# Performance work log

Measured on AMD Instinct MI355X. Metric: run time of the kernel, lower is better.

The kernel has to match this reference:

```python
import jax, jax.numpy as jnp
import numpy as np

IN_C = 256
INTER_C = 128  # in_channels // reduction_ratio


def setup_inputs() -> dict:
    key = jax.random.key(0)
    ks = jax.random.split(key, 9)
    s = 1.0 / np.sqrt(IN_C)
    si = 1.0 / np.sqrt(INTER_C)
    return {
        "x": jax.random.normal(ks[0], (8, IN_C, 64, 64), dtype=jnp.float32),
        "g_w": jax.random.uniform(ks[1], (INTER_C, IN_C), jnp.float32, -s, s),
        "g_b": jax.random.uniform(ks[2], (INTER_C,), jnp.float32, -s, s),
        "theta_w": jax.random.uniform(ks[3], (INTER_C, IN_C), jnp.float32, -s, s),
        "theta_b": jax.random.uniform(ks[4], (INTER_C,), jnp.float32, -s, s),
        "phi_w": jax.random.uniform(ks[5], (INTER_C, IN_C), jnp.float32, -s, s),
        "phi_b": jax.random.uniform(ks[6], (INTER_C,), jnp.float32, -s, s),
        "W_w": jax.random.uniform(ks[7], (IN_C, INTER_C), jnp.float32, -si, si),
        "W_b": jax.random.uniform(ks[8], (IN_C,), jnp.float32, -si, si),
    }


def _conv1x1(x, w, b):
    # x: [b, cin, h, w]; w: [cout, cin] -> [b, cout, h, w]
    return jnp.einsum('oc,bchw->bohw', w, x) + b[None, :, None, None]


def reference(x, g_w, g_b, theta_w, theta_b, phi_w, phi_b, W_w, W_b):
    b, c, h, w = x.shape
    n = h * w
    g_x = _conv1x1(x, g_w, g_b).reshape(b, INTER_C, n)        # [b, i, n]
    theta_x = _conv1x1(x, theta_w, theta_b).reshape(b, INTER_C, n)
    phi_x = _conv1x1(x, phi_w, phi_b).reshape(b, INTER_C, n)
    # f[b, q, k] = sum_i theta[b, i, q] * phi[b, i, k]
    f = jnp.einsum('biq,bik->bqk', theta_x, phi_x)            # [b, n, n]
    f_div_C = jax.nn.softmax(f, axis=-1)
    # y[b, q, i] = sum_k f_div_C[b, q, k] * g_x[b, i, k]
    y = jnp.einsum('bqk,bik->biq', f_div_C, g_x)              # [b, i, n]
    y = y.reshape(b, INTER_C, h, w)
    W_y = _conv1x1(y, W_w, W_b)
    return W_y + x
```

## Files before the change

### kernel.cpp

```cpp
#include <hip/hip_runtime.h>
#include <hip/hip_bf16.h>
#include <stdint.h>

#define NB 8
#define CIN 256
#define IC 128
#define NP 4096

typedef __attribute__((ext_vector_type(8))) short s8v;
typedef __attribute__((ext_vector_type(4))) short s4v;
typedef __attribute__((ext_vector_type(16))) float f16v;
typedef __attribute__((ext_vector_type(4))) float f4v;

#define MFMA32(a, b, c) __builtin_amdgcn_mfma_f32_32x32x16_bf16(a, b, c, 0, 0, 0)

__device__ __forceinline__ unsigned short f2bf(float f) {
  union { float f; unsigned int u; } v; v.f = f;
  unsigned int u = v.u;
  return (unsigned short)((u + 0x7FFFu + ((u >> 16) & 1u)) >> 16);
}

__device__ __forceinline__ unsigned short f2bf_h(float f) {
  __hip_bfloat16 h = __float2bfloat16(f);
  union { __hip_bfloat16 h; unsigned short u; } cv; cv.h = h;
  return cv.u;
}

__device__ __forceinline__ float bf2f(short s) {
  union { unsigned int u; float f; } cv;
  cv.u = ((unsigned int)(unsigned short)s) << 16;
  return cv.f;
}

typedef const unsigned int __attribute__((address_space(1))) gas_u32;
typedef unsigned int __attribute__((address_space(3))) las_u32;
__device__ __forceinline__ void gload_lds16(const void* g, void* l) {
  __builtin_amdgcn_global_load_lds((gas_u32*)g, (las_u32*)l, 16, 0, 0);
}

__global__ __launch_bounds__(256) void k_wprep(const float* __restrict__ thw,
    const float* __restrict__ phw, const float* __restrict__ gw,
    const float* __restrict__ Ww, unsigned short* __restrict__ wB) {
  const int g = blockIdx.x >> 5;
  const int base = (blockIdx.x & 31) * 1024 + threadIdx.x * 4;
  const float* src = (g == 0) ? thw : ((g == 1) ? phw : ((g == 2) ? gw : Ww));
  const float sc = (g == 0) ? 1.44269504f : 1.0f;
  const f4v v = *(const f4v*)(src + base);
  ushort4 u;
  u.x = f2bf(v[0] * sc); u.y = f2bf(v[1] * sc);
  u.z = f2bf(v[2] * sc); u.w = f2bf(v[3] * sc);
  *(ushort4*)(wB + g * 32768 + base) = u;
}

__global__ __launch_bounds__(256) void k_conv3(const float* __restrict__ x,
    const unsigned short* __restrict__ wB,
    const float* __restrict__ thb, const float* __restrict__ phb,
    const float* __restrict__ gb,
    unsigned short* __restrict__ Qg, unsigned short* __restrict__ Kg,
    unsigned short* __restrict__ Vtg) {
  __shared__ unsigned short X[64 * 256];
  __shared__ unsigned short T[64][72];
  const int t = threadIdx.x, lane = t & 63, wid = t >> 6;
  const int b = blockIdx.x & 7;
  const int p0 = (blockIdx.x >> 3) * 64;
  const int hl = lane >> 5;
  const float* xb = x + (size_t)b * CIN * NP + p0;
  const int cl = t >> 4;
  const int p4 = (t & 15) * 4;
  for (int sub = 0; sub < 4; ++sub) {
    const int c0 = sub * 64;
#pragma unroll
    for (int j = 0; j < 4; ++j) {
      const int cloc = cl + j * 16;
      const f4v v = *(const f4v*)(xb + (size_t)(c0 + cloc) * NP + p4);
      ushort4 u;
      u.x = f2bf(v[0]); u.y = f2bf(v[1]); u.z = f2bf(v[2]); u.w = f2bf(v[3]);
      *(ushort4*)&T[cloc][p4 ^ ((cloc & 7) * 8)] = u;
    }
    __syncthreads();
    const int p = t >> 2;
#pragma unroll
    for (int half = 0; half < 2; ++half) {
      const int cg = (t & 3) + half * 4;
      alignas(16) unsigned short outv[8];
#pragma unroll
      for (int k = 0; k < 8; ++k)
        outv[k] = T[cg * 8 + k][p ^ (k * 8)];
      const int cc = sub * 8 + cg;
      *(uint4*)&X[p * 256 + 8 * (cc ^ (2 * (p & 15)))] = *(const uint4*)outv;
    }
    __syncthreads();
  }
  const int orow = wid * 32 + (lane & 31);

  for (int mat = 0; mat < 3; ++mat) {
    const unsigned short* WB = wB + mat * 32768;
    const float* Bs = (mat == 0) ? thb : ((mat == 1) ? phb : gb);
    const float wsc = (mat == 0) ? 1.44269504f : 1.0f;
    s8v wf[16];
#pragma unroll
    for (int s = 0; s < 16; ++s)
      wf[s] = *(const s8v*)&WB[(size_t)orow * CIN + hl * 8 + 16 * s];
    float br[16];
#pragma unroll
    for (int r = 0; r < 16; ++r)
      br[r] = Bs[wid * 32 + (r & 3) + 8 * (r >> 2) + 4 * hl] * wsc;

#pragma unroll
    for (int nt = 0; nt < 2; ++nt) {
      const int p = (lane & 31) + nt * 32;
      f16v acc;
#pragma unroll
      for (int i = 0; i < 16; ++i) acc[i] = 0.f;
#pragma unroll
      for (int s = 0; s < 16; ++s) {
        const int cc0 = hl + 2 * s;
        const s8v xf = *(const s8v*)&X[p * 256 + 8 * (cc0 ^ (2 * (p & 15)))];
        acc = MFMA32(wf[s], xf, acc);
      }
      if (mat < 2) {
        unsigned short* G = ((mat == 0) ? Qg : Kg) + ((size_t)b * NP + p0 + p) * IC;
#pragma unroll
        for (int grp = 0; grp < 4; ++grp) {
          const int d0 = wid * 32 + 8 * grp + 4 * hl;
          ushort4 u;
          u.x = f2bf(acc[grp * 4 + 0] + br[grp * 4 + 0]);
          u.y = f2bf(acc[grp * 4 + 1] + br[grp * 4 + 1]);
          u.z = f2bf(acc[grp * 4 + 2] + br[grp * 4 + 2]);
          u.w = f2bf(acc[grp * 4 + 3] + br[grp * 4 + 3]);
          *(ushort4*)(G + d0) = u;
        }
      } else {
        unsigned short* G = Vtg + (size_t)b * IC * NP + p0 + p;
#pragma unroll
        for (int r = 0; r < 16; ++r) {
          const int row = wid * 32 + (r & 3) + 8 * (r >> 2) + 4 * hl;
          G[(size_t)row * NP] = f2bf(acc[r] + br[r]);
        }
      }
    }
  }
}

__global__ __launch_bounds__(256, 2) void k_attn(const unsigned short* __restrict__ Qg,
    const unsigned short* __restrict__ Kg, const unsigned short* __restrict__ Vtg,
    unsigned short* __restrict__ Opart, float2* __restrict__ stats) {
  __shared__ unsigned short Klds[2][64 * 128];
  __shared__ unsigned short Vlds[2][128 * 64];
  const int t = threadIdx.x, lane = t & 63, wid = t >> 6;
  const int bid = blockIdx.x;
  const int b = bid & 7;
  const int q0 = ((bid >> 3) & 31) * 128;
  const int half = bid >> 8;
  const int it0 = half * 32;
  const int hl = lane >> 5;
  const int q = q0 + wid * 32 + (lane & 31);
  const unsigned short* Qp = Qg + (size_t)b * NP * IC + (size_t)q * IC;
  s8v qf[8];
#pragma unroll
  for (int s = 0; s < 8; ++s)
    qf[s] = *(const s8v*)(Qp + hl * 8 + 16 * s);
  f16v oa[4];
#pragma unroll
  for (int dt = 0; dt < 4; ++dt)
#pragma unroll
    for (int i = 0; i < 16; ++i) oa[dt][i] = 0.f;
  float m = -3.0e38f, lsum = 0.f;
  const unsigned short* Kb = Kg + (size_t)b * NP * IC;
  const unsigned short* Vb = Vtg + (size_t)b * IC * NP;
  const int vrow_l = lane >> 3;
  const int vchunk = 8 * ((lane & 7) ^ vrow_l);

#pragma unroll
  for (int r = 0; r < 4; ++r) {
    const int ci = wid * 256 + r * 64 + lane;
    const int kv = ci >> 4, cc = ci & 15;
    gload_lds16(Kb + (size_t)(it0 * 64 + kv) * IC + 8 * (cc ^ (kv & 15)),
                (char*)&Klds[0][0] + wid * 4096 + r * 1024);
  }
#pragma unroll
  for (int r = 0; r < 4; ++r) {
    const int d = 32 * wid + 8 * r + vrow_l;
    gload_lds16(Vb + (size_t)d * NP + it0 * 64 + vchunk,
                (char*)&Vlds[0][0] + (32 * wid + 8 * r) * 128);
  }
  __syncthreads();

  for (int it = it0; it < it0 + 32; ++it) {
    const int cur = it & 1;
    const bool more = (it < it0 + 31);
    if (more) {
      const int kv0n = (it + 1) * 64;
#pragma unroll
      for (int r = 0; r < 4; ++r) {
        const int ci = wid * 256 + r * 64 + lane;
        const int kv = ci >> 4, cc = ci & 15;
        gload_lds16(Kb + (size_t)(kv0n + kv) * IC + 8 * (cc ^ (kv & 15)),
                    (char*)&Klds[cur ^ 1][0] + wid * 4096 + r * 1024);
      }
#pragma unroll
      for (int r = 0; r < 4; ++r) {
        const int d = 32 * wid + 8 * r + vrow_l;
        gload_lds16(Vb + (size_t)d * NP + kv0n + vchunk,
                    (char*)&Vlds[cur ^ 1][0] + (32 * wid + 8 * r) * 128);
      }
    }
    f16v st0a, st0b, st1a, st1b;
#pragma unroll
    for (int i = 0; i < 16; ++i) { st0a[i] = 0.f; st0b[i] = 0.f; st1a[i] = 0.f; st1b[i] = 0.f; }
    const int kva = lane & 31;
    __builtin_amdgcn_s_setprio(1);
#pragma unroll
    for (int s = 0; s < 8; s += 2) {
      const int cc0 = hl + 2 * s;
      const s8v ka0 = *(const s8v*)&Klds[cur][kva * 128 + 8 * (cc0 ^ (kva & 15))];
      const s8v kb0 = *(const s8v*)&Klds[cur][(kva + 32) * 128 + 8 * (cc0 ^ (kva & 15))];
      const s8v ka1 = *(const s8v*)&Klds[cur][kva * 128 + 8 * ((cc0 + 2) ^ (kva & 15))];
      const s8v kb1 = *(const s8v*)&Klds[cur][(kva + 32) * 128 + 8 * ((cc0 + 2) ^ (kva & 15))];
      st0a = MFMA32(ka0, qf[s], st0a);
      st1a = MFMA32(kb0, qf[s], st1a);
      st0b = MFMA32(ka1, qf[s + 1], st0b);
      st1b = MFMA32(kb1, qf[s + 1], st1b);
    }
    __builtin_amdgcn_s_setprio(0);
    f16v st0 = st0a + st0b;
    f16v st1 = st1a + st1b;
    float tm[16];
#pragma unroll
    for (int i = 0; i < 16; ++i) tm[i] = fmaxf(st0[i], st1[i]);
#pragma unroll
    for (int w = 8; w >= 1; w >>= 1)
#pragma unroll
      for (int i = 0; i < 16; ++i) if (i < w) tm[i] = fmaxf(tm[i], tm[i + w]);
    float pmax = fmaxf(tm[0], __shfl_xor(tm[0], 32));
    if (__any(pmax > m + 8.f)) {
      const float mn = fmaxf(m, pmax);
      const float sc = __builtin_amdgcn_exp2f(m - mn);
      m = mn;
      lsum *= sc;
#pragma unroll
      for (int dt = 0; dt < 4; ++dt)
#pragma unroll
        for (int i = 0; i < 16; ++i) oa[dt][i] *= sc;
    }
#pragma unroll
    for (int i = 0; i < 16; ++i) st0[i] = __builtin_amdgcn_exp2f(st0[i] - m);
#pragma unroll
    for (int i = 0; i < 16; ++i) st1[i] = __builtin_amdgcn_exp2f(st1[i] - m);
    float ts[16];
#pragma unroll
    for (int i = 0; i < 16; ++i) ts[i] = st0[i] + st1[i];
#pragma unroll
    for (int w = 8; w >= 1; w >>= 1)
#pragma unroll
      for (int i = 0; i < 16; ++i) if (i < w) ts[i] += ts[i + w];
    lsum += ts[0] + __shfl_xor(ts[0], 32);
    s8v pf0, pf1, pf2, pf3;
#pragma unroll
    for (int i = 0; i < 8; ++i) {
      pf0[i] = (short)f2bf_h(st0[i]);
      pf1[i] = (short)f2bf_h(st0[8 + i]);
      pf2[i] = (short)f2bf_h(st1[i]);
      pf3[i] = (short)f2bf_h(st1[8 + i]);
    }
    __builtin_amdgcn_s_setprio(1);
#pragma unroll
    for (int ks = 0; ks < 4; ++ks) {
      const s8v pcur = (ks == 0) ? pf0 : ((ks == 1) ? pf1 : ((ks == 2) ? pf2 : pf3));
      const int c0 = 2 * (ks & 1) + 4 * (ks >> 1);
#pragma unroll
      for (int dt = 0; dt < 4; ++dt) {
        const int d = dt * 32 + (lane & 31);
        const int dj = (lane & 31) & 7;
        const s4v va  = *(const s4v*)&Vlds[cur][d * 64 + 8 * (c0 ^ dj) + 4 * hl];
        const s4v vb2 = *(const s4v*)&Vlds[cur][d * 64 + 8 * ((c0 + 1) ^ dj) + 4 * hl];
        s8v vf;
        vf[0] = va[0]; vf[1] = va[1]; vf[2] = va[2]; vf[3] = va[3];
        vf[4] = vb2[0]; vf[5] = vb2[1]; vf[6] = vb2[2]; vf[7] = vb2[3];
        oa[dt] = MFMA32(vf, pcur, oa[dt]);
      }
    }
    __builtin_amdgcn_s_setprio(0);
    __syncthreads();
  }
  const float inv = 1.0f / lsum;
  unsigned short* Op = Opart + (size_t)half * NB * NP * IC + ((size_t)b * NP + q) * IC;
#pragma unroll
  for (int dt = 0; dt < 4; ++dt) {
#pragma unroll
    for (int grp = 0; grp < 4; ++grp) {
      const int d0 = dt * 32 + 8 * grp + 4 * hl;
      ushort4 u;
      u.x = f2bf_h(oa[dt][grp * 4 + 0] * inv);
      u.y = f2bf_h(oa[dt][grp * 4 + 1] * inv);
      u.z = f2bf_h(oa[dt][grp * 4 + 2] * inv);
      u.w = f2bf_h(oa[dt][grp * 4 + 3] * inv);
      *(ushort4*)(Op + d0) = u;
    }
  }
  if (hl == 0)
    stats[(size_t)half * NB * NP + (size_t)b * NP + q] = make_float2(m, lsum);
}

__global__ __launch_bounds__(256) void k_out(const unsigned short* __restrict__ Opart,
    const float2* __restrict__ stats,
    const unsigned short* __restrict__ WwB, const float* __restrict__ Wb,
    const float* __restrict__ x, float* __restrict__ out) {
  __shared__ unsigned short Y[64 * 128];
  const int t = threadIdx.x, lane = t & 63, wid = t >> 6;
  const int b = blockIdx.x & 7;
  const int p0 = (blockIdx.x >> 3) * 64;
  const int hl = lane >> 5;
  {
    const int p = t >> 2;
    const int quarter = t & 3;
    const int ihb = quarter * 32;
    const int gq = p0 + p;
    const float2 s0 = stats[(size_t)b * NP + gq];
    const float2 s1 = stats[(size_t)NB * NP + (size_t)b * NP + gq];
    const float mm = fmaxf(s0.x, s1.x);
    const float w0 = s0.y * exp2f(s0.x - mm);
    const float w1 = s1.y * exp2f(s1.x - mm);
    const float rinv = 1.0f / (w0 + w1);
    const float a0 = w0 * rinv, a1 = w1 * rinv;
    const unsigned short* P0 = Opart + ((size_t)b * NP + gq) * IC + ihb;
    const unsigned short* P1 = Opart + (size_t)NB * NP * IC + ((size_t)b * NP + gq) * IC + ihb;
#pragma unroll
    for (int c8 = 0; c8 < 4; ++c8) {
      const s8v v0 = *(const s8v*)(P0 + c8 * 8);
      const s8v v1 = *(const s8v*)(P1 + c8 * 8);
      alignas(16) unsigned short o[8];
#pragma unroll
      for (int j = 0; j < 8; ++j)
        o[j] = f2bf_h(a0 * bf2f(v0[j]) + a1 * bf2f(v1[j]));
      const int cc = quarter * 4 + c8;
      *(uint4*)&Y[p * 128 + 8 * (cc ^ (p & 15))] = *(const uint4*)o;
    }
  }
  __syncthreads();
  for (int mt = 0; mt < 2; ++mt) {
    const int orow = mt * 128 + wid * 32 + (lane & 31);
    s8v wf[8];
#pragma unroll
    for (int s = 0; s < 8; ++s)
      wf[s] = *(const s8v*)&WwB[(size_t)orow * IC + hl * 8 + 16 * s];
    float br[16];
#pragma unroll
    for (int r = 0; r < 16; ++r)
      br[r] = Wb[mt * 128 + wid * 32 + (r & 3) + 8 * (r >> 2) + 4 * hl];
#pragma unroll
    for (int nt = 0; nt < 2; ++nt) {
      const int p = (lane & 31) + nt * 32;
      f16v acc;
#pragma unroll
      for (int i = 0; i < 16; ++i) acc[i] = 0.f;
#pragma unroll
      for (int s = 0; s < 8; ++s) {
        const int cc0 = hl + 2 * s;
        const s8v yf = *(const s8v*)&Y[p * 128 + 8 * (cc0 ^ (p & 15))];
        acc = MFMA32(wf[s], yf, acc);
      }
      const size_t pidx = (size_t)b * CIN * NP + (size_t)(p0 + p);
#pragma unroll
      for (int r = 0; r < 16; ++r) {
        const int row = mt * 128 + wid * 32 + (r & 3) + 8 * (r >> 2) + 4 * hl;
        const size_t idx = pidx + (size_t)row * NP;
        out[idx] = acc[r] + br[r] + x[idx];
      }
    }
  }
}

extern "C" void kernel_launch(void* const* d_in, const int* in_sizes, int n_in,
                              void* d_out, int out_size, void* d_ws, size_t ws_size,
                              hipStream_t stream) {
  const float* x   = (const float*)d_in[0];
  const float* gw  = (const float*)d_in[1];
  const float* gb  = (const float*)d_in[2];
  const float* thw = (const float*)d_in[3];
  const float* thb = (const float*)d_in[4];
  const float* phw = (const float*)d_in[5];
  const float* phb = (const float*)d_in[6];
  const float* Ww  = (const float*)d_in[7];
  const float* Wb  = (const float*)d_in[8];
  float* out = (float*)d_out;

  unsigned short* ws  = (unsigned short*)d_ws;
  unsigned short* Opart = ws;
  unsigned short* Qg  = ws + 8388608;
  unsigned short* Kg  = Qg + 4194304;
  unsigned short* Vtg = Kg + 4194304;
  float2* stats = (float2*)(Vtg + 4194304);
  unsigned short* wB = Vtg + 4194304 + 262144;

  k_wprep<<<dim3(128), dim3(256), 0, stream>>>(thw, phw, gw, Ww, wB);
  k_conv3<<<dim3(512), dim3(256), 0, stream>>>(x, wB, thb, phb, gb,
                                               Qg, Kg, Vtg);
  k_attn<<<dim3(512), dim3(256), 0, stream>>>(Qg, Kg, Vtg, Opart, stats);
  k_out<<<dim3(512), dim3(256), 0, stream>>>(Opart, stats, wB + 98304, Wb, x, out);
}
```

Baseline: 143.3 us.

## Halve KV tile in attention kernel and stage V through padded LDS

Shrinks the attention kernel's KV tile from 64 to 32 keys per iteration, which halves the K and V LDS buffers, and raises the launch bound to three blocks per CU. V tiles are no longer loaded directly into LDS: each tile is read into registers, then written to a padded layout with a row stride of 34 elements, and that write is delayed until after the softmax. The aim is higher occupancy and overlap of the V global loads with compute. In exchange it doubles the number of loop iterations and barriers and adds register pressure. The padded rows are not 16-byte aligned, which may split LDS vector accesses or cause bank conflicts.

```diff
diff --git a/kernel.cpp b/kernel.cpp
--- a/kernel.cpp
+++ b/kernel.cpp
@@ -142,17 +142,17 @@
   }
 }
 
-__global__ __launch_bounds__(256, 2) void k_attn(const unsigned short* __restrict__ Qg,
+__global__ __launch_bounds__(256, 3) void k_attn(const unsigned short* __restrict__ Qg,
     const unsigned short* __restrict__ Kg, const unsigned short* __restrict__ Vtg,
     unsigned short* __restrict__ Opart, float2* __restrict__ stats) {
-  __shared__ unsigned short Klds[2][64 * 128];
-  __shared__ unsigned short Vlds[2][128 * 64];
+  __shared__ unsigned short Klds[2][32 * 128];
+  __shared__ unsigned short Vlds[2][128 * 34];
   const int t = threadIdx.x, lane = t & 63, wid = t >> 6;
   const int bid = blockIdx.x;
   const int b = bid & 7;
   const int q0 = ((bid >> 3) & 31) * 128;
   const int half = bid >> 8;
-  const int it0 = half * 32;
+  const int kvbase = half * 2048;
   const int hl = lane >> 5;
   const int q = q0 + wid * 32 + (lane & 31);
   const unsigned short* Qp = Qg + (size_t)b * NP * IC + (size_t)q * IC;
@@ -168,71 +168,64 @@
   float m = -3.0e38f, lsum = 0.f;
   const unsigned short* Kb = Kg + (size_t)b * NP * IC;
   const unsigned short* Vb = Vtg + (size_t)b * IC * NP;
-  const int vrow_l = lane >> 3;
-  const int vchunk = 8 * ((lane & 7) ^ vrow_l);
-
-#pragma unroll
-  for (int r = 0; r < 4; ++r) {
-    const int ci = wid * 256 + r * 64 + lane;
+  const int vd = t >> 2, vc = t & 3;
+
+  uint4 vreg[2];
+#pragma unroll
+  for (int r = 0; r < 2; ++r) {
+    const int ci = wid * 128 + r * 64 + lane;
     const int kv = ci >> 4, cc = ci & 15;
-    gload_lds16(Kb + (size_t)(it0 * 64 + kv) * IC + 8 * (cc ^ (kv & 15)),
-                (char*)&Klds[0][0] + wid * 4096 + r * 1024);
-  }
-#pragma unroll
-  for (int r = 0; r < 4; ++r) {
-    const int d = 32 * wid + 8 * r + vrow_l;
-    gload_lds16(Vb + (size_t)d * NP + it0 * 64 + vchunk,
-                (char*)&Vlds[0][0] + (32 * wid + 8 * r) * 128);
+    gload_lds16(Kb + (size_t)(kvbase + kv) * IC + 8 * (cc ^ (kv & 15)),
+                (char*)&Klds[0][0] + wid * 2048 + r * 1024);
+  }
+  {
+    const unsigned short* vs = Vb + kvbase + vc * 8;
+    vreg[0] = *(const uint4*)(vs + (size_t)vd * NP);
+    vreg[1] = *(const uint4*)(vs + (size_t)(vd + 64) * NP);
+    *(uint4*)&Vlds[0][vd * 34 + vc * 8] = vreg[0];
+    *(uint4*)&Vlds[0][(vd + 64) * 34 + vc * 8] = vreg[1];
   }
   __syncthreads();
 
-  for (int it = it0; it < it0 + 32; ++it) {
-    const int cur = it & 1;
-    const bool more = (it < it0 + 31);
+  for (int i = 0; i < 64; ++i) {
+    const int cur = i & 1;
+    const bool more = (i < 63);
     if (more) {
-      const int kv0n = (it + 1) * 64;
-#pragma unroll
-      for (int r = 0; r < 4; ++r) {
-        const int ci = wid * 256 + r * 64 + lane;
+      const int kv0n = kvbase + (i + 1) * 32;
+      const unsigned short* vs = Vb + kv0n + vc * 8;
+      vreg[0] = *(const uint4*)(vs + (size_t)vd * NP);
+      vreg[1] = *(const uint4*)(vs + (size_t)(vd + 64) * NP);
+#pragma unroll
+      for (int r = 0; r < 2; ++r) {
+        const int ci = wid * 128 + r * 64 + lane;
         const int kv = ci >> 4, cc = ci & 15;
         gload_lds16(Kb + (size_t)(kv0n + kv) * IC + 8 * (cc ^ (kv & 15)),
-                    (char*)&Klds[cur ^ 1][0] + wid * 4096 + r * 1024);
-      }
-#pragma unroll
-      for (int r = 0; r < 4; ++r) {
-        const int d = 32 * wid + 8 * r + vrow_l;
-        gload_lds16(Vb + (size_t)d * NP + kv0n + vchunk,
-                    (char*)&Vlds[cur ^ 1][0] + (32 * wid + 8 * r) * 128);
-      }
-    }
-    f16v st0a, st0b, st1a, st1b;
-#pragma unroll
-    for (int i = 0; i < 16; ++i) { st0a[i] = 0.f; st0b[i] = 0.f; st1a[i] = 0.f; st1b[i] = 0.f; }
+                    (char*)&Klds[cur ^ 1][0] + wid * 2048 + r * 1024);
+      }
+    }
+    f16v sa, sb;
+#pragma unroll
+    for (int ii = 0; ii < 16; ++ii) { sa[ii] = 0.f; sb[ii] = 0.f; }
     const int kva = lane & 31;
     __builtin_amdgcn_s_setprio(1);
 #pragma unroll
     for (int s = 0; s < 8; s += 2) {
       const int cc0 = hl + 2 * s;
       const s8v ka0 = *(const s8v*)&Klds[cur][kva * 128 + 8 * (cc0 ^ (kva & 15))];
-      const s8v kb0 = *(const s8v*)&Klds[cur][(kva + 32) * 128 + 8 * (cc0 ^ (kva & 15))];
       const s8v ka1 = *(const s8v*)&Klds[cur][kva * 128 + 8 * ((cc0 + 2) ^ (kva & 15))];
-      const s8v kb1 = *(const s8v*)&Klds[cur][(kva + 32) * 128 + 8 * ((cc0 + 2) ^ (kva & 15))];
-      st0a = MFMA32(ka0, qf[s], st0a);
-      st1a = MFMA32(kb0, qf[s], st1a);
-      st0b = MFMA32(ka1, qf[s + 1], st0b);
-      st1b = MFMA32(kb1, qf[s + 1], st1b);
+      sa = MFMA32(ka0, qf[s], sa);
+      sb = MFMA32(ka1, qf[s + 1], sb);
     }
     __builtin_amdgcn_s_setprio(0);
-    f16v st0 = st0a + st0b;
-    f16v st1 = st1a + st1b;
-    float tm[16];
-#pragma unroll
-    for (int i = 0; i < 16; ++i) tm[i] = fmaxf(st0[i], st1[i]);
-#pragma unroll
-    for (int w = 8; w >= 1; w >>= 1)
-#pragma unroll
-      for (int i = 0; i < 16; ++i) if (i < w) tm[i] = fmaxf(tm[i], tm[i + w]);
-    float pmax = fmaxf(tm[0], __shfl_xor(tm[0], 32));
+    f16v st = sa + sb;
+    float tm[8];
+#pragma unroll
+    for (int ii = 0; ii < 8; ++ii) tm[ii] = fmaxf(st[ii], st[ii + 8]);
+#pragma unroll
+    for (int w = 4; w >= 1; w >>= 1)
+#pragma unroll
+      for (int ii = 0; ii < 8; ++ii) if (ii < w) tm[ii] = fmaxf(tm[ii], tm[ii + w]);
+    const float pmax = fmaxf(tm[0], __shfl_xor(tm[0], 32));
     if (__any(pmax > m + 8.f)) {
       const float mn = fmaxf(m, pmax);
       const float sc = __builtin_amdgcn_exp2f(m - mn);
@@ -241,39 +234,38 @@
 #pragma unroll
       for (int dt = 0; dt < 4; ++dt)
 #pragma unroll
-        for (int i = 0; i < 16; ++i) oa[dt][i] *= sc;
-    }
-#pragma unroll
-    for (int i = 0; i < 16; ++i) st0[i] = __builtin_amdgcn_exp2f(st0[i] - m);
-#pragma unroll
-    for (int i = 0; i < 16; ++i) st1[i] = __builtin_amdgcn_exp2f(st1[i] - m);
-    float ts[16];
-#pragma unroll
-    for (int i = 0; i < 16; ++i) ts[i] = st0[i] + st1[i];
-#pragma unroll
-    for (int w = 8; w >= 1; w >>= 1)
-#pragma unroll
-      for (int i = 0; i < 16; ++i) if (i < w) ts[i] += ts[i + w];
+        for (int ii = 0; ii < 16; ++ii) oa[dt][ii] *= sc;
+    }
+#pragma unroll
+    for (int ii = 0; ii < 16; ++ii) st[ii] = __builtin_amdgcn_exp2f(st[ii] - m);
+    float ts[8];
+#pragma unroll
+    for (int ii = 0; ii < 8; ++ii) ts[ii] = st[ii] + st[ii + 8];
+#pragma unroll
+    for (int w = 4; w >= 1; w >>= 1)
+#pragma unroll
+      for (int ii = 0; ii < 8; ++ii) if (ii < w) ts[ii] += ts[ii + w];
     lsum += ts[0] + __shfl_xor(ts[0], 32);
-    s8v pf0, pf1, pf2, pf3;
-#pragma unroll
-    for (int i = 0; i < 8; ++i) {
-      pf0[i] = (short)f2bf_h(st0[i]);
-      pf1[i] = (short)f2bf_h(st0[8 + i]);
-      pf2[i] = (short)f2bf_h(st1[i]);
-      pf3[i] = (short)f2bf_h(st1[8 + i]);
+    s8v pf0, pf1;
+#pragma unroll
+    for (int ii = 0; ii < 8; ++ii) {
+      pf0[ii] = (short)f2bf_h(st[ii]);
+      pf1[ii] = (short)f2bf_h(st[8 + ii]);
+    }
+    if (more) {
+      *(uint4*)&Vlds[cur ^ 1][vd * 34 + vc * 8] = vreg[0];
+      *(uint4*)&Vlds[cur ^ 1][(vd + 64) * 34 + vc * 8] = vreg[1];
     }
     __builtin_amdgcn_s_setprio(1);
 #pragma unroll
-    for (int ks = 0; ks < 4; ++ks) {
-      const s8v pcur = (ks == 0) ? pf0 : ((ks == 1) ? pf1 : ((ks == 2) ? pf2 : pf3));
-      const int c0 = 2 * (ks & 1) + 4 * (ks >> 1);
+    for (int ks = 0; ks < 2; ++ks) {
+      const s8v pcur = (ks == 0) ? pf0 : pf1;
+      const int k0 = 16 * ks + 4 * hl;
 #pragma unroll
       for (int dt = 0; dt < 4; ++dt) {
         const int d = dt * 32 + (lane & 31);
-        const int dj = (lane & 31) & 7;
-        const s4v va  = *(const s4v*)&Vlds[cur][d * 64 + 8 * (c0 ^ dj) + 4 * hl];
-        const s4v vb2 = *(const s4v*)&Vlds[cur][d * 64 + 8 * ((c0 + 1) ^ dj) + 4 * hl];
+        const s4v va  = *(const s4v*)&Vlds[cur][d * 34 + k0];
+        const s4v vb2 = *(const s4v*)&Vlds[cur][d * 34 + k0 + 8];
         s8v vf;
         vf[0] = va[0]; vf[1] = va[1]; vf[2] = va[2]; vf[3] = va[3];
         vf[4] = vb2[0]; vf[5] = vb2[1]; vf[6] = vb2[2]; vf[7] = vb2[3];
```

Result: slower. 149.4 us (+4.2%).
